# Kernel optimization log

Hardware: AMD Instinct MI355X
Metric: run time of the kernel (lower is better)

The kernel has to match this reference:

```python
import jax, jax.numpy as jnp
import numpy as np

EPS = 1e-5

def mean_variance_norm(x):
    # x: [b, c, h, w]; per-(b,c) instance norm over spatial, unbiased var (torch default)
    b, c, h, w = x.shape
    xf = x.reshape(b, c, h * w)
    mean = xf.mean(axis=2)
    var = xf.var(axis=2, ddof=1) + EPS
    std = jnp.sqrt(var)
    return (x - mean[:, :, None, None]) / std[:, :, None, None]

def conv1x1(x, w, b):
    # w: [out_c, in_c], b: [out_c]
    return jnp.einsum('oc,bchw->bohw', w, x) + b[None, :, None, None]

def setup_inputs() -> dict:
    key = jax.random.key(0)
    ks = jax.random.split(key, 10)
    b, C, H, W = 4, 512, 64, 64
    content = jax.random.normal(ks[0], (b, C, H, W), dtype=jnp.float32)
    style = jax.random.normal(ks[1], (b, C, H, W), dtype=jnp.float32)
    def w_(k, o, i):
        return jax.random.normal(k, (o, i), dtype=jnp.float32) * 0.02
    def b_(k, o):
        return jax.random.normal(k, (o,), dtype=jnp.float32) * 0.02
    return {
        'content': content, 'style': style,
        'f_w': w_(ks[2], C, C), 'f_b': b_(ks[3], C),
        'g_w': w_(ks[4], C, C), 'g_b': b_(ks[5], C),
        'h_w': w_(ks[6], C, C), 'h_b': b_(ks[7], C),
        'out_w': w_(ks[8], C, C), 'out_b': b_(ks[9], C),
    }

def reference(content, style, f_w, f_b, g_w, g_b, h_w, h_b, out_w, out_b):
    b, C, h, w = content.shape
    F = conv1x1(mean_variance_norm(content), f_w, f_b)   # [b,C,h,w]
    G = conv1x1(mean_variance_norm(style), g_w, g_b)     # [b,C,hg,wg]
    H = conv1x1(style, h_w, h_b)                          # [b,C,hg,wg]
    # spatial <= max_sample, so no subsampling branch
    Gf = G.reshape(b, C, -1)                              # [b,C,M]
    Hf = H.reshape(b, C, -1)                              # [b,C,M]
    Ff = F.reshape(b, C, -1)                              # [b,C,N]
    S = jnp.einsum('bcn,bcm->bnm', Ff, Gf)                # [b,N,M]
    S = jax.nn.softmax(S, axis=-1)
    styled = jnp.einsum('bcm,bnm->bcn', Hf, S)            # [b,C,N]
    styled = styled.reshape(b, C, h, w)
    return conv1x1(styled, out_w, out_b)
```

## Files before the change

kernel.cpp:

```cpp
#include <hip/hip_runtime.h>
#include <hip/hip_bf16.h>

typedef _Float16 f16;
typedef __attribute__((ext_vector_type(8))) _Float16 half8;
typedef __attribute__((ext_vector_type(4))) _Float16 half4;
typedef __attribute__((ext_vector_type(4))) float f32x4;

#define AS1 __attribute__((address_space(1)))
#define AS3 __attribute__((address_space(3)))

constexpr int CH  = 512;
constexpr int NSP = 4096;
constexpr int NB  = 4;

#define VM8  asm volatile("s_waitcnt vmcnt(8)"  ::: "memory")
#define VM0  asm volatile("s_waitcnt vmcnt(0)"  ::: "memory")
#define BARS do { __builtin_amdgcn_s_barrier(); asm volatile("" ::: "memory"); } while (0)

__device__ __forceinline__ void gload_lds16(const void* g, void* l) {
    __builtin_amdgcn_global_load_lds((const AS1 void*)g, (AS3 void*)l, 16, 0, 0);
}

__global__ void stats_kernel(const float* __restrict__ c_, const float* __restrict__ s_,
                             float* __restrict__ stats)
{
    int row = blockIdx.x;
    const float* p = ((row < NB*CH) ? c_ : s_) + (size_t)(row & (NB*CH - 1)) * NSP;
    float s = 0.f, ss = 0.f;
    for (int i = threadIdx.x; i < NSP/4; i += 256) {
        float4 v = ((const float4*)p)[i];
        s  += v.x + v.y + v.z + v.w;
        ss += v.x*v.x + v.y*v.y + v.z*v.z + v.w*v.w;
    }
    #pragma unroll
    for (int off = 32; off; off >>= 1) { s += __shfl_down(s, off); ss += __shfl_down(ss, off); }
    __shared__ float r1[4], r2[4];
    if ((threadIdx.x & 63) == 0) { r1[threadIdx.x >> 6] = s; r2[threadIdx.x >> 6] = ss; }
    __syncthreads();
    if (threadIdx.x == 0) {
        s = r1[0]+r1[1]+r1[2]+r1[3]; ss = r2[0]+r2[1]+r2[2]+r2[3];
        float mean = s * (1.f/NSP);
        float var  = (ss - (float)NSP*mean*mean) * (1.f/(NSP-1));
        int base = (row < NB*CH) ? 0 : 2*NB*CH;
        int r = row & (NB*CH - 1);
        stats[base + r] = mean;
        stats[base + NB*CH + r] = rsqrtf(var + 1e-5f);
    }
}

__global__ void effw_kernel(const float* __restrict__ fw, const float* __restrict__ fb,
                            const float* __restrict__ gw, const float* __restrict__ gb,
                            const float* __restrict__ hw, const float* __restrict__ ow,
                            const float* __restrict__ stats,
                            f16* __restrict__ fw_e, float* __restrict__ fb_e,
                            f16* __restrict__ gw_e, float* __restrict__ gb_e,
                            f16* __restrict__ hw_h, f16* __restrict__ ow_h)
{
    int o = blockIdx.x, b = blockIdx.y, mode = blockIdx.z, t = threadIdx.x;
    if (mode >= 2) {
        if (b != 0) return;
        const float* srcw = (mode == 2) ? hw : ow;
        f16* dstw = (mode == 2) ? hw_h : ow_h;
        for (int c = t; c < CH; c += 128) dstw[o*CH + c] = (f16)srcw[o*CH + c];
        return;
    }
    const float* w  = mode ? gw : fw;
    const float* st = stats + (mode ? 2*NB*CH : 0);
    f16* we = mode ? gw_e : fw_e;
    float part = 0.f;
    for (int c = t; c < CH; c += 128) {
        float mn = st[b*CH + c], is = st[NB*CH + b*CH + c];
        float wv = w[o*CH + c];
        we[((size_t)b*CH + o)*CH + c] = (f16)(wv * is);
        part += wv * mn * is;
    }
    #pragma unroll
    for (int off = 32; off; off >>= 1) part += __shfl_down(part, off);
    __shared__ float rr[2];
    if ((t & 63) == 0) rr[t >> 6] = part;
    __syncthreads();
    if (t == 0) (mode ? gb_e : fb_e)[b*CH + o] = (mode ? gb : fb)[o] - (rr[0] + rr[1]);
}

__global__ void transpose_f16_kernel(const float* __restrict__ content, const float* __restrict__ style,
                                     f16* __restrict__ content_t, f16* __restrict__ style_t)
{
    int b = blockIdx.z & 3, is_style = blockIdx.z >> 2;
    const float* src = (is_style ? style : content) + (size_t)b * CH * NSP;
    f16* dst = (is_style ? style_t : content_t) + (size_t)b * NSP * CH;
    int c0 = blockIdx.y * 64, n0 = blockIdx.x * 64;
    __shared__ f16 tile[64][72];
    int t = threadIdx.x;
    #pragma unroll
    for (int i = 0; i < 4; i++) {
        int idx = t + i*256;
        int cr = idx >> 4, n4 = (idx & 15) * 4;
        float4 v = *(const float4*)(src + (size_t)(c0+cr)*NSP + n0 + n4);
        tile[cr][n4+0] = (f16)v.x; tile[cr][n4+1] = (f16)v.y;
        tile[cr][n4+2] = (f16)v.z; tile[cr][n4+3] = (f16)v.w;
    }
    __syncthreads();
    int nr = t >> 2, seg = (t & 3) * 16;
    __align__(16) f16 out_v[16];
    #pragma unroll
    for (int j = 0; j < 16; j++) out_v[j] = tile[seg + j][nr];
    f16* dp = dst + (size_t)(n0+nr)*CH + c0 + seg;
    *(int4*)dp = ((int4*)out_v)[0];
    *(int4*)(dp + 8) = ((int4*)out_v)[1];
}

template<int MODE>
__global__ __launch_bounds__(256)
void gemm_kernel(const f16* __restrict__ W, long wstrideb,
                 const f16* __restrict__ Xt, long xstrideb,
                 const float* __restrict__ bias, long bstrideb,
                 void* __restrict__ Y, long ystrideb,
                 int K, long ostride)
{
    const int z = blockIdx.z;
    W    += (size_t)z * wstrideb;
    Xt   += (size_t)z * xstrideb;
    bias += (size_t)z * bstrideb;
    const int m0 = blockIdx.y * 128, n0 = blockIdx.x * 128;
    const int t = threadIdx.x, wave = t >> 6, lane = t & 63;
    const int l15 = lane & 15, l4 = lane >> 4;
    const int wm = (wave >> 1) * 64, wn = (wave & 1) * 64;

    __shared__ __align__(16) f16 Al[2][8192];
    __shared__ __align__(16) f16 Bl[2][8192];

    f32x4 acc[4][4] = {};

    auto stage = [&](int bufi, int kk) {
        #pragma unroll
        for (int j = 0; j < 4; j++) {
            int L  = ((wave*4 + j)*64 + lane) * 16;
            int SL = L ^ (((L >> 7) & 7) << 4);
            int row = SL >> 7, seg = (SL & 127) >> 1;
            gload_lds16(W  + (size_t)(m0 + row)*K + kk + seg, &Al[bufi][L >> 1]);
            gload_lds16(Xt + (size_t)(n0 + row)*K + kk + seg, &Bl[bufi][L >> 1]);
        }
    };

    const int nks = K >> 6;
    stage(0, 0);
    for (int ks = 0; ks < nks; ks++) {
        int bufi = ks & 1;
        if (ks < nks-1) { stage(bufi ^ 1, (ks + 1) * 64); VM8; }
        else            { VM0; }
        BARS;
        #pragma unroll
        for (int kb = 0; kb < 2; kb++) {
            half8 a[4], bb[4];
            #pragma unroll
            for (int i = 0; i < 4; i++) {
                int ab = (wm + i*16 + l15)*128 + kb*64 + l4*16;
                ab ^= ((ab >> 7) & 7) << 4;
                a[i] = *(const half8*)&Al[bufi][ab >> 1];
                int bby = (wn + i*16 + l15)*128 + kb*64 + l4*16;
                bby ^= ((bby >> 7) & 7) << 4;
                bb[i] = *(const half8*)&Bl[bufi][bby >> 1];
            }
            #pragma unroll
            for (int i = 0; i < 4; i++)
                #pragma unroll
                for (int jj = 0; jj < 4; jj++)
                    acc[i][jj] = __builtin_amdgcn_mfma_f32_16x16x32_f16(a[i], bb[jj], acc[i][jj], 0, 0, 0);
        }
        BARS;
    }

    #pragma unroll
    for (int i = 0; i < 4; i++) {
        const int ob = m0 + wm + i*16 + l4*4;
        f32x4 bv = *(const f32x4*)(bias + ob);
        #pragma unroll
        for (int jj = 0; jj < 4; jj++) {
            const int n = n0 + wn + jj*16 + l15;
            f32x4 v = acc[i][jj];
            v[0] += bv[0]; v[1] += bv[1]; v[2] += bv[2]; v[3] += bv[3];
            if constexpr (MODE == 0) {
                f16* Yb = (f16*)Y + (size_t)z * ystrideb;
                half4 pk; pk[0]=(f16)v[0]; pk[1]=(f16)v[1]; pk[2]=(f16)v[2]; pk[3]=(f16)v[3];
                *(half4*)(Yb + (size_t)n * ostride + ob) = pk;
            } else if constexpr (MODE == 1) {
                f16* Yb = (f16*)Y + (size_t)z * ystrideb;
                #pragma unroll
                for (int r = 0; r < 4; r++) Yb[(size_t)(ob + r) * ostride + n] = (f16)v[r];
            } else {
                float* Yf = (float*)Y + (size_t)z * ystrideb;
                #pragma unroll
                for (int r = 0; r < 4; r++) Yf[(size_t)(ob + r) * ostride + n] = v[r];
            }
        }
    }
}

template<int TPB, int NCT>
__global__ __launch_bounds__(256)
void gemm_att_kernel(const f16* __restrict__ W, long wstrideb,
                     const f16* __restrict__ Xt, long xstrideb,
                     f16* __restrict__ Y, long ystrideb,
                     int K, long ostride)
{
    const int T = gridDim.x;
    const int bid = blockIdx.x;
    const int tile = (bid & 7) * (T >> 3) + (bid >> 3);
    const int z = tile / TPB, rem = tile - z * TPB;
    const int mt = rem / NCT, nt = rem - mt * NCT;
    W  += (size_t)z * wstrideb;
    Xt += (size_t)z * xstrideb;
    f16* Yb = Y + (size_t)z * ystrideb;
    const int m0 = mt * 128, n0 = nt * 128;

    const int t = threadIdx.x, wave = t >> 6, lane = t & 63;
    const int l15 = lane & 15, l4 = lane >> 4;
    const int wm = (wave >> 1) * 64, wn = (wave & 1) * 64;

    __shared__ __align__(16) f16 Al[8192];
    __shared__ __align__(16) f16 Bl[8192];

    f32x4 acc[4][4] = {};

    auto stage = [&](int kk) {
        #pragma unroll
        for (int j = 0; j < 4; j++) {
            int L  = ((wave*4 + j)*64 + lane) * 16;
            int SL = L ^ (((L >> 7) & 7) << 4);
            int row = SL >> 7, seg = (SL & 127) >> 1;
            gload_lds16(W  + (size_t)(m0 + row)*K + kk + seg, &Al[L >> 1]);
            gload_lds16(Xt + (size_t)(n0 + row)*K + kk + seg, &Bl[L >> 1]);
        }
    };

    const int nks = K >> 6;
    for (int ks = 0; ks < nks; ks++) {
        stage(ks * 64);
        VM0; BARS;
        #pragma unroll
        for (int kb = 0; kb < 2; kb++) {
            half8 a[4], bb[4];
            #pragma unroll
            for (int i = 0; i < 4; i++) {
                int ab = (wm + i*16 + l15)*128 + kb*64 + l4*16;
                ab ^= ((ab >> 7) & 7) << 4;
                a[i] = *(const half8*)&Al[ab >> 1];
                int bby = (wn + i*16 + l15)*128 + kb*64 + l4*16;
                bby ^= ((bby >> 7) & 7) << 4;
                bb[i] = *(const half8*)&Bl[bby >> 1];
            }
            #pragma unroll
            for (int i = 0; i < 4; i++)
                #pragma unroll
                for (int jj = 0; jj < 4; jj++)
                    acc[i][jj] = __builtin_amdgcn_mfma_f32_16x16x32_f16(a[i], bb[jj], acc[i][jj], 0, 0, 0);
        }
        BARS;
    }

    #pragma unroll
    for (int i = 0; i < 4; i++) {
        const int ob = m0 + wm + i*16 + l4*4;
        #pragma unroll
        for (int jj = 0; jj < 4; jj++) {
            const int ncol = n0 + wn + jj*16 + l15;
            #pragma unroll
            for (int r = 0; r < 4; r++)
                Yb[(size_t)(ob + r) * ostride + ncol] = (f16)acc[i][jj][r];
        }
    }
}

__global__ __launch_bounds__(256)
void softmax_kernel(f16* __restrict__ S, int nrows)
{
    int row = blockIdx.x * 4 + (threadIdx.x >> 6);
    if (row >= nrows) return;
    int lane = threadIdx.x & 63;
    f16* p = S + (size_t)row * NSP + lane * 8;

    half8 v[8];
    #pragma unroll
    for (int j = 0; j < 8; j++) v[j] = *(const half8*)(p + j * 512);

    float mx = -1e30f;
    #pragma unroll
    for (int j = 0; j < 8; j++)
        #pragma unroll
        for (int e = 0; e < 8; e++) mx = fmaxf(mx, (float)v[j][e]);
    #pragma unroll
    for (int off = 32; off; off >>= 1) mx = fmaxf(mx, __shfl_xor(mx, off));

    float ex[64];
    float s = 0.f;
    #pragma unroll
    for (int j = 0; j < 8; j++)
        #pragma unroll
        for (int e = 0; e < 8; e++) {
            float x = __expf((float)v[j][e] - mx);
            ex[j*8 + e] = x; s += x;
        }
    #pragma unroll
    for (int off = 32; off; off >>= 1) s += __shfl_xor(s, off);
    float inv = 1.0f / s;

    #pragma unroll
    for (int j = 0; j < 8; j++) {
        half8 o;
        #pragma unroll
        for (int e = 0; e < 8; e++) o[e] = (f16)(ex[j*8 + e] * inv);
        *(half8*)(p + j * 512) = o;
    }
}

extern "C" void kernel_launch(void* const* d_in, const int* in_sizes, int n_in,
                              void* d_out, int out_size, void* d_ws, size_t ws_size,
                              hipStream_t stream)
{
    const float* content = (const float*)d_in[0];
    const float* style   = (const float*)d_in[1];
    const float* f_w = (const float*)d_in[2];
    const float* f_b = (const float*)d_in[3];
    const float* g_w = (const float*)d_in[4];
    const float* g_b = (const float*)d_in[5];
    const float* h_w = (const float*)d_in[6];
    const float* h_b = (const float*)d_in[7];
    const float* o_w = (const float*)d_in[8];
    const float* o_b = (const float*)d_in[9];

    char* ws = (char*)d_ws;
    size_t off = 0;
    auto alloc = [&](size_t bytes) -> void* {
        void* p = ws + off;
        off += (bytes + 255) & ~(size_t)255;
        return p;
    };
    float* stats = (float*)alloc(4 * NB*CH * 4);
    float* zeros = (float*)alloc(NSP * 4);
    f16* fw_e = (f16*)alloc((size_t)NB*CH*CH*2);
    f16* gw_e = (f16*)alloc((size_t)NB*CH*CH*2);
    f16* hw_h = (f16*)alloc((size_t)CH*CH*2);
    f16* ow_h = (f16*)alloc((size_t)CH*CH*2);
    float* fb_e = (float*)alloc((size_t)NB*CH*4);
    float* gb_e = (float*)alloc((size_t)NB*CH*4);
    f16* content_t = (f16*)alloc((size_t)NB*NSP*CH*2);
    f16* style_t   = (f16*)alloc((size_t)NB*NSP*CH*2);
    f16* F_t = (f16*)alloc((size_t)NB*NSP*CH*2);
    f16* G_t = (f16*)alloc((size_t)NB*NSP*CH*2);
    f16* H_  = (f16*)alloc((size_t)NB*CH*NSP*2);
    f16* styled_t = content_t;

    size_t s_plane = (size_t)NSP * NSP;
    bool all4 = (off + 4 * s_plane * 2 <= ws_size);
    f16* S16 = (f16*)alloc((all4 ? 4 : 1) * s_plane * 2);
    if (off > ws_size) return;

    hipMemsetAsync(zeros, 0, NSP * 4, stream);
    stats_kernel<<<dim3(2*NB*CH), dim3(256), 0, stream>>>(content, style, stats);
    effw_kernel<<<dim3(CH, NB, 4), dim3(128), 0, stream>>>(f_w, f_b, g_w, g_b, h_w, o_w, stats,
                                                           fw_e, fb_e, gw_e, gb_e, hw_h, ow_h);
    transpose_f16_kernel<<<dim3(NSP/64, CH/64, NB*2), dim3(256), 0, stream>>>(content, style, content_t, style_t);

    gemm_kernel<0><<<dim3(NSP/128, CH/128, NB), dim3(256), 0, stream>>>(
        fw_e, (long)CH*CH, content_t, (long)NSP*CH, fb_e, (long)CH, (void*)F_t, (long)NSP*CH, CH, (long)CH);
    gemm_kernel<0><<<dim3(NSP/128, CH/128, NB), dim3(256), 0, stream>>>(
        gw_e, (long)CH*CH, style_t, (long)NSP*CH, gb_e, (long)CH, (void*)G_t, (long)NSP*CH, CH, (long)CH);
    gemm_kernel<1><<<dim3(NSP/128, CH/128, NB), dim3(256), 0, stream>>>(
        hw_h, 0L, style_t, (long)NSP*CH, h_b, 0L, (void*)H_, (long)CH*NSP, CH, (long)NSP);

    if (all4) {
        gemm_att_kernel<1024,32><<<dim3(NB*1024), dim3(256), 0, stream>>>(
            F_t, (long)NSP*CH, G_t, (long)NSP*CH, S16, (long)s_plane, CH, (long)NSP);
        softmax_kernel<<<dim3(NB*NSP/4), dim3(256), 0, stream>>>(S16, NB*NSP);
        gemm_att_kernel<128,4><<<dim3(NB*128), dim3(256), 0, stream>>>(
            S16, (long)s_plane, H_, (long)CH*NSP, styled_t, (long)NSP*CH, NSP, (long)CH);
    } else {
        for (int b = 0; b < NB; b++) {
            gemm_att_kernel<1024,32><<<dim3(1024), dim3(256), 0, stream>>>(
                F_t + (size_t)b*NSP*CH, 0L, G_t + (size_t)b*NSP*CH, 0L,
                S16, 0L, CH, (long)NSP);
            softmax_kernel<<<dim3(NSP/4), dim3(256), 0, stream>>>(S16, NSP);
            gemm_att_kernel<128,4><<<dim3(128), dim3(256), 0, stream>>>(
                S16, 0L, H_ + (size_t)b*CH*NSP, 0L,
                styled_t + (size_t)b*NSP*CH, 0L, NSP, (long)CH);
        }
    }

    gemm_kernel<2><<<dim3(NSP/128, CH/128, NB), dim3(256), 0, stream>>>(
        ow_h, 0L, styled_t, (long)NSP*CH, o_b, 0L, d_out, (long)CH*NSP, CH, (long)NSP);
}
```

Before: 320.5 us.

## Fuse stats into transpose, merge three convs, split-K the PV GEMM

Per-channel sum and sum-of-squares are now computed inside the transpose kernel with atomics, and mean/rstd are derived in effw_kernel, so the separate stats pass over the inputs is gone. The F, G and H 1x1 convs run as a single launch of 1536 tiles instead of three launches of 512. The PV GEMM, which had only 512 blocks with K=4096, is split along K into two halves writing into the now-free F_t and G_t buffers, followed by a reduce kernel, to give more parallelism. This adds float atomics (nondeterministic summation order), an extra f16 round-trip on the partial sums, and one more kernel launch.

```diff
diff --git a/kernel.cpp b/kernel.cpp
--- a/kernel.cpp
+++ b/kernel.cpp
@@ -21,37 +21,54 @@
     __builtin_amdgcn_global_load_lds((const AS1 void*)g, (AS3 void*)l, 16, 0, 0);
 }
 
-__global__ void stats_kernel(const float* __restrict__ c_, const float* __restrict__ s_,
-                             float* __restrict__ stats)
-{
-    int row = blockIdx.x;
-    const float* p = ((row < NB*CH) ? c_ : s_) + (size_t)(row & (NB*CH - 1)) * NSP;
-    float s = 0.f, ss = 0.f;
-    for (int i = threadIdx.x; i < NSP/4; i += 256) {
-        float4 v = ((const float4*)p)[i];
-        s  += v.x + v.y + v.z + v.w;
-        ss += v.x*v.x + v.y*v.y + v.z*v.z + v.w*v.w;
-    }
-    #pragma unroll
-    for (int off = 32; off; off >>= 1) { s += __shfl_down(s, off); ss += __shfl_down(ss, off); }
-    __shared__ float r1[4], r2[4];
-    if ((threadIdx.x & 63) == 0) { r1[threadIdx.x >> 6] = s; r2[threadIdx.x >> 6] = ss; }
+__global__ void transpose_f16_kernel(const float* __restrict__ content, const float* __restrict__ style,
+                                     f16* __restrict__ content_t, f16* __restrict__ style_t,
+                                     float* __restrict__ raw)
+{
+    int b = blockIdx.z & 3, is_style = blockIdx.z >> 2;
+    const float* src = (is_style ? style : content) + (size_t)b * CH * NSP;
+    f16* dst = (is_style ? style_t : content_t) + (size_t)b * NSP * CH;
+    int c0 = blockIdx.y * 64, n0 = blockIdx.x * 64;
+    __shared__ f16 tile[64][72];
+    int t = threadIdx.x;
+    #pragma unroll
+    for (int i = 0; i < 4; i++) {
+        int idx = t + i*256;
+        int cr = idx >> 4, n4 = (idx & 15) * 4;
+        float4 v = *(const float4*)(src + (size_t)(c0+cr)*NSP + n0 + n4);
+        tile[cr][n4+0] = (f16)v.x; tile[cr][n4+1] = (f16)v.y;
+        tile[cr][n4+2] = (f16)v.z; tile[cr][n4+3] = (f16)v.w;
+    }
     __syncthreads();
-    if (threadIdx.x == 0) {
-        s = r1[0]+r1[1]+r1[2]+r1[3]; ss = r2[0]+r2[1]+r2[2]+r2[3];
-        float mean = s * (1.f/NSP);
-        float var  = (ss - (float)NSP*mean*mean) * (1.f/(NSP-1));
-        int base = (row < NB*CH) ? 0 : 2*NB*CH;
-        int r = row & (NB*CH - 1);
-        stats[base + r] = mean;
-        stats[base + NB*CH + r] = rsqrtf(var + 1e-5f);
-    }
+    {
+        int row = t >> 2, seg = (t & 3) * 16;
+        float s1 = 0.f, s2 = 0.f;
+        #pragma unroll
+        for (int j = 0; j < 16; j++) {
+            float x = (float)tile[row][seg + j];
+            s1 += x; s2 += x * x;
+        }
+        s1 += __shfl_down(s1, 2, 4); s1 += __shfl_down(s1, 1, 4);
+        s2 += __shfl_down(s2, 2, 4); s2 += __shfl_down(s2, 1, 4);
+        if ((t & 3) == 0) {
+            int si = is_style * 2 * NB * CH + b * CH + c0 + row;
+            atomicAdd(&raw[si], s1);
+            atomicAdd(&raw[si + NB * CH], s2);
+        }
+    }
+    int nr = t >> 2, seg = (t & 3) * 16;
+    __align__(16) f16 out_v[16];
+    #pragma unroll
+    for (int j = 0; j < 16; j++) out_v[j] = tile[seg + j][nr];
+    f16* dp = dst + (size_t)(n0+nr)*CH + c0 + seg;
+    *(int4*)dp = ((int4*)out_v)[0];
+    *(int4*)(dp + 8) = ((int4*)out_v)[1];
 }
 
 __global__ void effw_kernel(const float* __restrict__ fw, const float* __restrict__ fb,
                             const float* __restrict__ gw, const float* __restrict__ gb,
                             const float* __restrict__ hw, const float* __restrict__ ow,
-                            const float* __restrict__ stats,
+                            const float* __restrict__ raw,
                             f16* __restrict__ fw_e, float* __restrict__ fb_e,
                             f16* __restrict__ gw_e, float* __restrict__ gb_e,
                             f16* __restrict__ hw_h, f16* __restrict__ ow_h)
@@ -65,11 +82,14 @@
         return;
     }
     const float* w  = mode ? gw : fw;
-    const float* st = stats + (mode ? 2*NB*CH : 0);
+    const float* rw = raw + (mode ? 2*NB*CH : 0);
     f16* we = mode ? gw_e : fw_e;
     float part = 0.f;
     for (int c = t; c < CH; c += 128) {
-        float mn = st[b*CH + c], is = st[NB*CH + b*CH + c];
+        float s1 = rw[b*CH + c], s2 = rw[NB*CH + b*CH + c];
+        float mn = s1 * (1.f/NSP);
+        float var = (s2 - (float)NSP*mn*mn) * (1.f/(NSP-1));
+        float is = rsqrtf(var + 1e-5f);
         float wv = w[o*CH + c];
         we[((size_t)b*CH + o)*CH + c] = (f16)(wv * is);
         part += wv * mn * is;
@@ -82,31 +102,85 @@
     if (t == 0) (mode ? gb_e : fb_e)[b*CH + o] = (mode ? gb : fb)[o] - (rr[0] + rr[1]);
 }
 
-__global__ void transpose_f16_kernel(const float* __restrict__ content, const float* __restrict__ style,
-                                     f16* __restrict__ content_t, f16* __restrict__ style_t)
-{
-    int b = blockIdx.z & 3, is_style = blockIdx.z >> 2;
-    const float* src = (is_style ? style : content) + (size_t)b * CH * NSP;
-    f16* dst = (is_style ? style_t : content_t) + (size_t)b * NSP * CH;
-    int c0 = blockIdx.y * 64, n0 = blockIdx.x * 64;
-    __shared__ f16 tile[64][72];
-    int t = threadIdx.x;
+__global__ __launch_bounds__(256)
+void conv3_kernel(const f16* __restrict__ fw_e, const float* __restrict__ fb_e,
+                  const f16* __restrict__ gw_e, const float* __restrict__ gb_e,
+                  const f16* __restrict__ hw_h, const float* __restrict__ h_b,
+                  const f16* __restrict__ content_t, const f16* __restrict__ style_t,
+                  f16* __restrict__ F_t, f16* __restrict__ G_t, f16* __restrict__ H_)
+{
+    const int T = gridDim.x;
+    const int bid = blockIdx.x;
+    const int tile = (bid & 7) * (T >> 3) + (bid >> 3);
+    const int zz = tile >> 7, rem = tile & 127;
+    const int mt = rem >> 5, nt = rem & 31;
+    const int kind = zz >> 2, b = zz & 3;
+
+    const f16* W; const float* bias; const f16* Xt; f16* Y;
+    if (kind == 0)      { W = fw_e + (size_t)b*CH*CH; bias = fb_e + b*CH; Xt = content_t + (size_t)b*NSP*CH; Y = F_t + (size_t)b*NSP*CH; }
+    else if (kind == 1) { W = gw_e + (size_t)b*CH*CH; bias = gb_e + b*CH; Xt = style_t + (size_t)b*NSP*CH; Y = G_t + (size_t)b*NSP*CH; }
+    else                { W = hw_h;                    bias = h_b;         Xt = style_t + (size_t)b*NSP*CH; Y = H_ + (size_t)b*CH*NSP; }
+
+    const int m0 = mt * 128, n0 = nt * 128;
+    const int t = threadIdx.x, wave = t >> 6, lane = t & 63;
+    const int l15 = lane & 15, l4 = lane >> 4;
+    const int wm = (wave >> 1) * 64, wn = (wave & 1) * 64;
+
+    __shared__ __align__(16) f16 Al[8192];
+    __shared__ __align__(16) f16 Bl[8192];
+
+    f32x4 acc[4][4] = {};
+
+    for (int ks = 0; ks < CH/64; ks++) {
+        const int kk = ks * 64;
+        #pragma unroll
+        for (int j = 0; j < 4; j++) {
+            int L  = ((wave*4 + j)*64 + lane) * 16;
+            int SL = L ^ (((L >> 7) & 7) << 4);
+            int row = SL >> 7, seg = (SL & 127) >> 1;
+            gload_lds16(W  + (size_t)(m0 + row)*CH + kk + seg, &Al[L >> 1]);
+            gload_lds16(Xt + (size_t)(n0 + row)*CH + kk + seg, &Bl[L >> 1]);
+        }
+        VM0; BARS;
+        #pragma unroll
+        for (int kb = 0; kb < 2; kb++) {
+            half8 a[4], bb[4];
+            #pragma unroll
+            for (int i = 0; i < 4; i++) {
+                int ab = (wm + i*16 + l15)*128 + kb*64 + l4*16;
+                ab ^= ((ab >> 7) & 7) << 4;
+                a[i] = *(const half8*)&Al[ab >> 1];
+                int bby = (wn + i*16 + l15)*128 + kb*64 + l4*16;
+                bby ^= ((bby >> 7) & 7) << 4;
+                bb[i] = *(const half8*)&Bl[bby >> 1];
+            }
+            #pragma unroll
+            for (int i = 0; i < 4; i++)
+                #pragma unroll
+                for (int jj = 0; jj < 4; jj++)
+                    acc[i][jj] = __builtin_amdgcn_mfma_f32_16x16x32_f16(a[i], bb[jj], acc[i][jj], 0, 0, 0);
+        }
+        BARS;
+    }
+
     #pragma unroll
     for (int i = 0; i < 4; i++) {
-        int idx = t + i*256;
-        int cr = idx >> 4, n4 = (idx & 15) * 4;
-        float4 v = *(const float4*)(src + (size_t)(c0+cr)*NSP + n0 + n4);
-        tile[cr][n4+0] = (f16)v.x; tile[cr][n4+1] = (f16)v.y;
-        tile[cr][n4+2] = (f16)v.z; tile[cr][n4+3] = (f16)v.w;
-    }
-    __syncthreads();
-    int nr = t >> 2, seg = (t & 3) * 16;
-    __align__(16) f16 out_v[16];
-    #pragma unroll
-    for (int j = 0; j < 16; j++) out_v[j] = tile[seg + j][nr];
-    f16* dp = dst + (size_t)(n0+nr)*CH + c0 + seg;
-    *(int4*)dp = ((int4*)out_v)[0];
-    *(int4*)(dp + 8) = ((int4*)out_v)[1];
+        const int ob = m0 + wm + i*16 + l4*4;
+        f32x4 bv = *(const f32x4*)(bias + ob);
+        #pragma unroll
+        for (int jj = 0; jj < 4; jj++) {
+            const int n = n0 + wn + jj*16 + l15;
+            f32x4 v = acc[i][jj];
+            v[0] += bv[0]; v[1] += bv[1]; v[2] += bv[2]; v[3] += bv[3];
+            if (kind < 2) {
+                half4 pk; pk[0]=(f16)v[0]; pk[1]=(f16)v[1]; pk[2]=(f16)v[2]; pk[3]=(f16)v[3];
+                *(half4*)(Y + (size_t)n * CH + ob) = pk;
+            } else {
+                #pragma unroll
+                for (int r = 0; r < 4; r++) Y[(size_t)(ob + r) * NSP + n] = (f16)v[r];
+            }
+        }
+    }
 }
 
 template<int MODE>
@@ -179,19 +253,9 @@
             const int n = n0 + wn + jj*16 + l15;
             f32x4 v = acc[i][jj];
             v[0] += bv[0]; v[1] += bv[1]; v[2] += bv[2]; v[3] += bv[3];
-            if constexpr (MODE == 0) {
-                f16* Yb = (f16*)Y + (size_t)z * ystrideb;
-                half4 pk; pk[0]=(f16)v[0]; pk[1]=(f16)v[1]; pk[2]=(f16)v[2]; pk[3]=(f16)v[3];
-                *(half4*)(Yb + (size_t)n * ostride + ob) = pk;
-            } else if constexpr (MODE == 1) {
-                f16* Yb = (f16*)Y + (size_t)z * ystrideb;
-                #pragma unroll
-                for (int r = 0; r < 4; r++) Yb[(size_t)(ob + r) * ostride + n] = (f16)v[r];
-            } else {
-                float* Yf = (float*)Y + (size_t)z * ystrideb;
-                #pragma unroll
-                for (int r = 0; r < 4; r++) Yf[(size_t)(ob + r) * ostride + n] = v[r];
-            }
+            float* Yf = (float*)Y + (size_t)z * ystrideb;
+            #pragma unroll
+            for (int r = 0; r < 4; r++) Yf[(size_t)(ob + r) * ostride + n] = v[r];
         }
     }
 }
@@ -222,7 +286,9 @@
 
     f32x4 acc[4][4] = {};
 
-    auto stage = [&](int kk) {
+    const int nks = K >> 6;
+    for (int ks = 0; ks < nks; ks++) {
+        const int kk = ks * 64;
         #pragma unroll
         for (int j = 0; j < 4; j++) {
             int L  = ((wave*4 + j)*64 + lane) * 16;
@@ -231,11 +297,6 @@
             gload_lds16(W  + (size_t)(m0 + row)*K + kk + seg, &Al[L >> 1]);
             gload_lds16(Xt + (size_t)(n0 + row)*K + kk + seg, &Bl[L >> 1]);
         }
-    };
-
-    const int nks = K >> 6;
-    for (int ks = 0; ks < nks; ks++) {
-        stage(ks * 64);
         VM0; BARS;
         #pragma unroll
         for (int kb = 0; kb < 2; kb++) {
@@ -269,6 +330,93 @@
                 Yb[(size_t)(ob + r) * ostride + ncol] = (f16)acc[i][jj][r];
         }
     }
+}
+
+template<int NCT>
+__global__ __launch_bounds__(256)
+void pv_split_kernel(const f16* __restrict__ S, long sstride,
+                     const f16* __restrict__ Hm, long hstride,
+                     f16* __restrict__ P0, f16* __restrict__ P1,
+                     long pstride, int Khalf)
+{
+    const int T = gridDim.x;
+    const int bid = blockIdx.x;
+    const int tile = (bid & 7) * (T >> 3) + (bid >> 3);
+    const int TPB = 32 * NCT;
+    const int sp = tile / (NB * TPB);
+    int rem = tile - sp * NB * TPB;
+    const int z = rem / TPB; rem -= z * TPB;
+    const int mt = rem / NCT, nt = rem - mt * NCT;
+    const f16* W  = S  + (size_t)z * sstride + (size_t)sp * Khalf;
+    const f16* Xt = Hm + (size_t)z * hstride + (size_t)sp * Khalf;
+    f16* Yb = (sp ? P1 : P0) + (size_t)z * pstride;
+    const int m0 = mt * 128, n0 = nt * 128;
+
+    const int t = threadIdx.x, wave = t >> 6, lane = t & 63;
+    const int l15 = lane & 15, l4 = lane >> 4;
+    const int wm = (wave >> 1) * 64, wn = (wave & 1) * 64;
+
+    __shared__ __align__(16) f16 Al[8192];
+    __shared__ __align__(16) f16 Bl[8192];
+
+    f32x4 acc[4][4] = {};
+
+    const int nks = Khalf >> 6;
+    for (int ks = 0; ks < nks; ks++) {
+        const int kk = ks * 64;
+        #pragma unroll
+        for (int j = 0; j < 4; j++) {
+            int L  = ((wave*4 + j)*64 + lane) * 16;
+            int SL = L ^ (((L >> 7) & 7) << 4);
+            int row = SL >> 7, seg = (SL & 127) >> 1;
+            gload_lds16(W  + (size_t)(m0 + row)*NSP + kk + seg, &Al[L >> 1]);
+            gload_lds16(Xt + (size_t)(n0 + row)*NSP + kk + seg, &Bl[L >> 1]);
+        }
+        VM0; BARS;
+        #pragma unroll
+        for (int kb = 0; kb < 2; kb++) {
+            half8 a[4], bb[4];
+            #pragma unroll
+            for (int i = 0; i < 4; i++) {
+                int ab = (wm + i*16 + l15)*128 + kb*64 + l4*16;
+                ab ^= ((ab >> 7) & 7) << 4;
+                a[i] = *(const half8*)&Al[ab >> 1];
+                int bby = (wn + i*16 + l15)*128 + kb*64 + l4*16;
+                bby ^= ((bby >> 7) & 7) << 4;
+                bb[i] = *(const half8*)&Bl[bby >> 1];
+            }
+            #pragma unroll
+            for (int i = 0; i < 4; i++)
+                #pragma unroll
+                for (int jj = 0; jj < 4; jj++)
+                    acc[i][jj] = __builtin_amdgcn_mfma_f32_16x16x32_f16(a[i], bb[jj], acc[i][jj], 0, 0, 0);
+        }
+        BARS;
+    }
+
+    #pragma unroll
+    for (int i = 0; i < 4; i++) {
+        const int ob = m0 + wm + i*16 + l4*4;
+        #pragma unroll
+        for (int jj = 0; jj < 4; jj++) {
+            const int ncol = n0 + wn + jj*16 + l15;
+            #pragma unroll
+            for (int r = 0; r < 4; r++)
+                Yb[(size_t)(ob + r) * CH + ncol] = (f16)acc[i][jj][r];
+        }
+    }
+}
+
+__global__ __launch_bounds__(256)
+void reduce_pv_kernel(const f16* __restrict__ p0, const f16* __restrict__ p1, f16* __restrict__ out)
+{
+    size_t i = ((size_t)blockIdx.x * 256 + threadIdx.x) * 8;
+    half8 a = *(const half8*)(p0 + i);
+    half8 b = *(const half8*)(p1 + i);
+    half8 o;
+    #pragma unroll
+    for (int e = 0; e < 8; e++) o[e] = (f16)((float)a[e] + (float)b[e]);
+    *(half8*)(out + i) = o;
 }
 
 __global__ __launch_bounds__(256)
@@ -335,8 +483,7 @@
         off += (bytes + 255) & ~(size_t)255;
         return p;
     };
-    float* stats = (float*)alloc(4 * NB*CH * 4);
-    float* zeros = (float*)alloc(NSP * 4);
+    float* raw = (float*)alloc(4 * NB*CH * 4);
     f16* fw_e = (f16*)alloc((size_t)NB*CH*CH*2);
     f16* gw_e = (f16*)alloc((size_t)NB*CH*CH*2);
     f16* hw_h = (f16*)alloc((size_t)CH*CH*2);
@@ -355,25 +502,21 @@
     f16* S16 = (f16*)alloc((all4 ? 4 : 1) * s_plane * 2);
     if (off > ws_size) return;
 
-    hipMemsetAsync(zeros, 0, NSP * 4, stream);
-    stats_kernel<<<dim3(2*NB*CH), dim3(256), 0, stream>>>(content, style, stats);
-    effw_kernel<<<dim3(CH, NB, 4), dim3(128), 0, stream>>>(f_w, f_b, g_w, g_b, h_w, o_w, stats,
+    hipMemsetAsync(raw, 0, 4 * NB*CH * 4, stream);
+    transpose_f16_kernel<<<dim3(NSP/64, CH/64, NB*2), dim3(256), 0, stream>>>(
+        content, style, content_t, style_t, raw);
+    effw_kernel<<<dim3(CH, NB, 4), dim3(128), 0, stream>>>(f_w, f_b, g_w, g_b, h_w, o_w, raw,
                                                            fw_e, fb_e, gw_e, gb_e, hw_h, ow_h);
-    transpose_f16_kernel<<<dim3(NSP/64, CH/64, NB*2), dim3(256), 0, stream>>>(content, style, content_t, style_t);
-
-    gemm_kernel<0><<<dim3(NSP/128, CH/128, NB), dim3(256), 0, stream>>>(
-        fw_e, (long)CH*CH, content_t, (long)NSP*CH, fb_e, (long)CH, (void*)F_t, (long)NSP*CH, CH, (long)CH);
-    gemm_kernel<0><<<dim3(NSP/128, CH/128, NB), dim3(256), 0, stream>>>(
-        gw_e, (long)CH*CH, style_t, (long)NSP*CH, gb_e, (long)CH, (void*)G_t, (long)NSP*CH, CH, (long)CH);
-    gemm_kernel<1><<<dim3(NSP/128, CH/128, NB), dim3(256), 0, stream>>>(
-        hw_h, 0L, style_t, (long)NSP*CH, h_b, 0L, (void*)H_, (long)CH*NSP, CH, (long)NSP);
+    conv3_kernel<<<dim3(12*128), dim3(256), 0, stream>>>(
+        fw_e, fb_e, gw_e, gb_e, hw_h, h_b, content_t, style_t, F_t, G_t, H_);
 
     if (all4) {
         gemm_att_kernel<1024,32><<<dim3(NB*1024), dim3(256), 0, stream>>>(
             F_t, (long)NSP*CH, G_t, (long)NSP*CH, S16, (long)s_plane, CH, (long)NSP);
         softmax_kernel<<<dim3(NB*NSP/4), dim3(256), 0, stream>>>(S16, NB*NSP);
-        gemm_att_kernel<128,4><<<dim3(NB*128), dim3(256), 0, stream>>>(
-            S16, (long)s_plane, H_, (long)CH*NSP, styled_t, (long)NSP*CH, NSP, (long)CH);
+        pv_split_kernel<4><<<dim3(1024), dim3(256), 0, stream>>>(
+            S16, (long)s_plane, H_, (long)CH*NSP, F_t, G_t, (long)NSP*CH, NSP/2);
+        reduce_pv_kernel<<<dim3((int)((size_t)NB*NSP*CH/2048)), dim3(256), 0, stream>>>(F_t, G_t, styled_t);
     } else {
         for (int b = 0; b < NB; b++) {
             gemm_att_kernel<1024,32><<<dim3(1024), dim3(256), 0, stream>>>(
```

New measurement: 311.4 us. 2.9% less time.
